# Performance work log

Hardware: AMD Instinct MI355X
Metric: run time of the kernel (lower is better)

## Reference

```python
import jax, jax.numpy as jnp
import numpy as np

B, S, D, H, FACTOR = 1, 2048, 1024, 16, 16
HD = D // H


def setup_inputs() -> dict:
    key = jax.random.key(0)
    ks = jax.random.split(key, 9)
    s = 1.0 / np.sqrt(D)
    u = lambda k, shape: jax.random.uniform(k, shape, jnp.float32, -s, s)
    return {
        "x": jax.random.normal(ks[0], (B, S, D), jnp.float32),
        "Wq": u(ks[1], (D, D)), "bq": u(ks[2], (D,)),
        "Wk": u(ks[3], (D, D)), "bk": u(ks[4], (D,)),
        "Wv": u(ks[5], (D, D)), "bv": u(ks[6], (D,)),
        "Wo": u(ks[7], (D, D)), "bo": u(ks[8], (D,)),
    }


def reference(x, Wq, bq, Wk, bk, Wv, bv, Wo, bo):
    b, s, d = x.shape
    h, hd = H, HD
    # projections -> [b, h, s, hd]
    q = (x @ Wq + bq).reshape(b, s, h, hd).transpose(0, 2, 1, 3)
    k = (x @ Wk + bk).reshape(b, s, h, hd).transpose(0, 2, 1, 3)
    v = (x @ Wv + bv).reshape(b, s, h, hd).transpose(0, 2, 1, 3)
    # dense scores [b, h, s, s]
    scores = jnp.einsum('bhqd,bhkd->bhqk', q, k) / np.sqrt(hd).astype(np.float32)
    # top-k along last dim, scatter into zeros (non-topk entries stay 0, as in torch code)
    vals, idx = jax.lax.top_k(scores, FACTOR)  # [b,h,s,FACTOR]
    flat_scores = scores.reshape(-1, s)
    rows = jnp.arange(flat_scores.shape[0])[:, None]
    sparse = jnp.zeros_like(flat_scores).at[rows, idx.reshape(-1, FACTOR)].set(
        vals.reshape(-1, FACTOR)).reshape(scores.shape)
    attn = jax.nn.softmax(sparse, axis=-1)  # softmax over sparse scores incl. zeros
    out = jnp.einsum('bhqk,bhkd->bhqd', attn, v)
    out = out.transpose(0, 2, 1, 3).reshape(b, s, d)
    return out @ Wo + bo
```

## Files before the change

kernel.cpp:

```cpp
#include <hip/hip_runtime.h>
#include <stdint.h>

constexpr int SEQ  = 2048;
constexpr int DIM  = 1024;
constexpr int NH   = 16;
constexpr int HDIM = 64;
constexpr int TOPK = 16;
constexpr int CAP  = 96;
constexpr int CST  = 97;
constexpr int QR   = 32;

typedef unsigned short bf16_t;
typedef __attribute__((ext_vector_type(8))) short bf16x8;
typedef __attribute__((ext_vector_type(4))) float f32x4;
typedef unsigned long long u64;

__device__ __forceinline__ int swzc(int col, int row) { return col ^ ((row & 7) << 3); }

__device__ __forceinline__ float bf2f(bf16_t b) {
  return __uint_as_float(((unsigned)b) << 16);
}
__device__ __forceinline__ bf16_t f2bf(float f) {
  unsigned u = __float_as_uint(f);
  unsigned r = u + 0x7fffu + ((u >> 16) & 1u);
  return (bf16_t)(r >> 16);
}
__device__ __forceinline__ f32x4 zero4() {
  f32x4 z; z[0] = 0.f; z[1] = 0.f; z[2] = 0.f; z[3] = 0.f; return z;
}
__device__ __forceinline__ void gload_lds16(const bf16_t* g, bf16_t* l) {
  __builtin_amdgcn_global_load_lds(
      (const __attribute__((address_space(1))) void*)g,
      (__attribute__((address_space(3))) void*)l, 16, 0, 0);
}
__device__ __forceinline__ unsigned ordf(float f) {
  unsigned b = __float_as_uint(f);
  return (b & 0x80000000u) ? ~b : (b | 0x80000000u);
}
__device__ __forceinline__ float iordf(unsigned u) {
  unsigned b = (u & 0x80000000u) ? (u ^ 0x80000000u) : ~u;
  return __uint_as_float(b);
}

__global__ void prep_kernel(const float* __restrict__ x, bf16_t* __restrict__ xb,
                            const float* __restrict__ W0, const float* __restrict__ W1,
                            const float* __restrict__ W2, const float* __restrict__ W3,
                            bf16_t* __restrict__ T0, bf16_t* __restrict__ T1,
                            bf16_t* __restrict__ T2, bf16_t* __restrict__ T3) {
  const int z = blockIdx.z;
  if (z == 4) {
    int bl = blockIdx.y * 32 + blockIdx.x;
    int tt = threadIdx.y * 32 + threadIdx.x;
    int i = (bl * 256 + tt) * 8;
    float4 v0 = *reinterpret_cast<const float4*>(x + i);
    float4 v1 = *reinterpret_cast<const float4*>(x + i + 4);
    bf16x8 o;
    o[0] = (short)f2bf(v0.x); o[1] = (short)f2bf(v0.y);
    o[2] = (short)f2bf(v0.z); o[3] = (short)f2bf(v0.w);
    o[4] = (short)f2bf(v1.x); o[5] = (short)f2bf(v1.y);
    o[6] = (short)f2bf(v1.z); o[7] = (short)f2bf(v1.w);
    *reinterpret_cast<bf16x8*>(xb + i) = o;
    return;
  }
  const float* W = (z == 0) ? W0 : (z == 1) ? W1 : (z == 2) ? W2 : W3;
  bf16_t* WT = (z == 0) ? T0 : (z == 1) ? T1 : (z == 2) ? T2 : T3;
  __shared__ float tile[32][33];
  int tx = threadIdx.x, ty = threadIdx.y;
  int bx = blockIdx.x * 32, by = blockIdx.y * 32;
#pragma unroll
  for (int i = 0; i < 4; ++i)
    tile[ty + i * 8][tx] = W[(by + ty + i * 8) * DIM + bx + tx];
  __syncthreads();
#pragma unroll
  for (int i = 0; i < 4; ++i)
    WT[(bx + ty + i * 8) * DIM + by + tx] = f2bf(tile[tx][ty + i * 8]);
}

__global__ __launch_bounds__(256) void gemm_qkv(const bf16_t* __restrict__ A,
                                                const bf16_t* __restrict__ B0,
                                                const bf16_t* __restrict__ B1,
                                                const bf16_t* __restrict__ B2,
                                                const float* __restrict__ c0,
                                                const float* __restrict__ c1,
                                                const float* __restrict__ c2,
                                                bf16_t* __restrict__ o0,
                                                bf16_t* __restrict__ o1,
                                                bf16_t* __restrict__ o2,
                                                float* __restrict__ sumv) {
  __shared__ __align__(16) bf16_t As[2][128 * 64];
  __shared__ __align__(16) bf16_t Bs[2][128 * 64];
  const int t = threadIdx.x;
  const int which = blockIdx.x >> 3;
  const bf16_t* Bt = (which == 0) ? B0 : (which == 1) ? B1 : B2;
  const float* bias = (which == 0) ? c0 : (which == 1) ? c1 : c2;
  bf16_t* out = (which == 0) ? o0 : (which == 1) ? o1 : o2;
  const int bm0 = blockIdx.y * 128, bn0 = (blockIdx.x & 7) * 128;
  const int w = t >> 6, lane = t & 63, lr = lane & 15, lg = lane >> 4;
  const int wm = w >> 1, wn = w & 1;
  const int srow = t >> 3;
  const int scol = swzc((t & 7) * 8, srow);
  const int ldst = srow * 64 + (t & 7) * 8;
  const int rsw = (lr & 7) << 3;

  f32x4 acc[4][4];
#pragma unroll
  for (int m = 0; m < 4; ++m)
#pragma unroll
    for (int n = 0; n < 4; ++n) acc[m][n] = zero4();

#define STAGE_G(buf, kt)                                                             \
  do {                                                                               \
    _Pragma("unroll") for (int i_ = 0; i_ < 4; ++i_) {                               \
      gload_lds16(A + (size_t)(bm0 + i_ * 32 + srow) * DIM + (kt) * 64 + scol,       \
                  &As[buf][i_ * 32 * 64 + ldst]);                                    \
      gload_lds16(Bt + (size_t)(bn0 + i_ * 32 + srow) * DIM + (kt) * 64 + scol,      \
                  &Bs[buf][i_ * 32 * 64 + ldst]);                                    \
    }                                                                                \
  } while (0)

  STAGE_G(0, 0);
  __syncthreads();

  for (int s = 0; s < 16; ++s) {
    const int cur = s & 1;
    if (s < 15) STAGE_G(cur ^ 1, s + 1);
    bf16x8 a[4][2], b[4][2];
#pragma unroll
    for (int m = 0; m < 4; ++m)
#pragma unroll
      for (int kk = 0; kk < 2; ++kk)
        a[m][kk] = *reinterpret_cast<const bf16x8*>(
            &As[cur][(wm * 64 + m * 16 + lr) * 64 + ((kk * 32 + lg * 8) ^ rsw)]);
#pragma unroll
    for (int n = 0; n < 4; ++n)
#pragma unroll
      for (int kk = 0; kk < 2; ++kk)
        b[n][kk] = *reinterpret_cast<const bf16x8*>(
            &Bs[cur][(wn * 64 + n * 16 + lr) * 64 + ((kk * 32 + lg * 8) ^ rsw)]);
#pragma unroll
    for (int m = 0; m < 4; ++m)
#pragma unroll
      for (int n = 0; n < 4; ++n)
#pragma unroll
        for (int kk = 0; kk < 2; ++kk)
          acc[m][n] = __builtin_amdgcn_mfma_f32_16x16x32_bf16(a[m][kk], b[n][kk],
                                                              acc[m][n], 0, 0, 0);
    __syncthreads();
  }
#undef STAGE_G

#pragma unroll
  for (int n = 0; n < 4; ++n) {
    int col = bn0 + wn * 64 + n * 16 + lr;
    float bv = bias[col];
    float colsum = 0.f;
#pragma unroll
    for (int m = 0; m < 4; ++m)
#pragma unroll
      for (int r = 0; r < 4; ++r) {
        int row = bm0 + wm * 64 + m * 16 + lg * 4 + r;
        bf16_t rb = f2bf(acc[m][n][r] + bv);
        out[(size_t)row * DIM + col] = rb;
        if (which == 2) colsum += bf2f(rb);
      }
    if (which == 2) atomicAdd(&sumv[col], colsum);
  }
}

__global__ __launch_bounds__(256) void gemm_wo(const bf16_t* __restrict__ A,
                                               const bf16_t* __restrict__ Bt,
                                               const float* __restrict__ bias,
                                               float* __restrict__ out) {
  __shared__ __align__(16) bf16_t As[2][128 * 64];
  __shared__ __align__(16) bf16_t Bs[2][64 * 64];
  const int t = threadIdx.x;
  const int bm0 = blockIdx.y * 128, bn0 = blockIdx.x * 64;
  const int w = t >> 6, lane = t & 63, lr = lane & 15, lg = lane >> 4;
  const int wm = w >> 1, wn = w & 1;
  const int srow = t >> 3;
  const int scol = swzc((t & 7) * 8, srow);
  const int ldst = srow * 64 + (t & 7) * 8;
  const int rsw = (lr & 7) << 3;

  f32x4 acc[4][2];
#pragma unroll
  for (int m = 0; m < 4; ++m)
#pragma unroll
    for (int n = 0; n < 2; ++n) acc[m][n] = zero4();

#define STAGE_W(buf, kt)                                                             \
  do {                                                                               \
    _Pragma("unroll") for (int i_ = 0; i_ < 4; ++i_)                                 \
      gload_lds16(A + (size_t)(bm0 + i_ * 32 + srow) * DIM + (kt) * 64 + scol,       \
                  &As[buf][i_ * 32 * 64 + ldst]);                                    \
    _Pragma("unroll") for (int i_ = 0; i_ < 2; ++i_)                                 \
      gload_lds16(Bt + (size_t)(bn0 + i_ * 32 + srow) * DIM + (kt) * 64 + scol,      \
                  &Bs[buf][i_ * 32 * 64 + ldst]);                                    \
  } while (0)

  STAGE_W(0, 0);
  __syncthreads();

  for (int s = 0; s < 16; ++s) {
    const int cur = s & 1;
    if (s < 15) STAGE_W(cur ^ 1, s + 1);
    bf16x8 a[4][2], b[2][2];
#pragma unroll
    for (int m = 0; m < 4; ++m)
#pragma unroll
      for (int kk = 0; kk < 2; ++kk)
        a[m][kk] = *reinterpret_cast<const bf16x8*>(
            &As[cur][(wm * 64 + m * 16 + lr) * 64 + ((kk * 32 + lg * 8) ^ rsw)]);
#pragma unroll
    for (int n = 0; n < 2; ++n)
#pragma unroll
      for (int kk = 0; kk < 2; ++kk)
        b[n][kk] = *reinterpret_cast<const bf16x8*>(
            &Bs[cur][(wn * 32 + n * 16 + lr) * 64 + ((kk * 32 + lg * 8) ^ rsw)]);
#pragma unroll
    for (int m = 0; m < 4; ++m)
#pragma unroll
      for (int n = 0; n < 2; ++n)
#pragma unroll
        for (int kk = 0; kk < 2; ++kk)
          acc[m][n] = __builtin_amdgcn_mfma_f32_16x16x32_bf16(a[m][kk], b[n][kk],
                                                              acc[m][n], 0, 0, 0);
    __syncthreads();
  }
#undef STAGE_W

#pragma unroll
  for (int n = 0; n < 2; ++n) {
    int col = bn0 + wn * 32 + n * 16 + lr;
    float bv = bias[col];
#pragma unroll
    for (int m = 0; m < 4; ++m)
#pragma unroll
      for (int r = 0; r < 4; ++r) {
        int row = bm0 + wm * 64 + m * 16 + lg * 4 + r;
        out[(size_t)row * DIM + col] = acc[m][n][r] + bv;
      }
  }
}

#define LOADK(buf, kc)                                                              \
  do {                                                                              \
    _Pragma("unroll") for (int n_ = 0; n_ < 4; ++n_)                                \
      _Pragma("unroll") for (int k_ = 0; k_ < 2; ++k_)                              \
        kf[buf][n_][k_] = *reinterpret_cast<const bf16x8*>(                         \
            kp + (size_t)((kc) * 64 + n_ * 16 + lr) * DIM + k_ * 32 + lg * 8);      \
  } while (0)

__global__ __launch_bounds__(256, 2) void attn_kernel(const bf16_t* __restrict__ q,
                                                      const bf16_t* __restrict__ k,
                                                      const bf16_t* __restrict__ v,
                                                      const float* __restrict__ sumv,
                                                      bf16_t* __restrict__ op) {
  __shared__ float CM[QR * 33];
  __shared__ float Tsh[QR];
  __shared__ float zsh[QR];
  __shared__ int   cnt[QR];
  __shared__ float cval[QR * CST];
  __shared__ unsigned short cidx[QR * CST];

  const int t = threadIdx.x;
  const int lin = blockIdx.x;
  const int xcd = lin & 7, ixd = lin >> 3;
  const int h = xcd * 2 + (ixd >> 6), qt = ixd & 63;
  const int w = t >> 6, lane = t & 63, lr = lane & 15, lg = lane >> 4;

  const bf16_t* qp = q + (size_t)(qt * QR) * DIM + h * HDIM;
  const bf16_t* kp = k + h * HDIM;

  bf16x8 aq[2][2];
#pragma unroll
  for (int m = 0; m < 2; ++m)
#pragma unroll
    for (int kk = 0; kk < 2; ++kk)
      aq[m][kk] = *reinterpret_cast<const bf16x8*>(
          qp + (size_t)(m * 16 + lr) * DIM + kk * 32 + lg * 8);

  bf16x8 kf[2][4][2];

  LOADK(0, w * 8);
#pragma unroll
  for (int i = 0; i < 8; ++i) {
    if (i < 7) LOADK((i + 1) & 1, w * 8 + i + 1);
    const int cur = i & 1;
    f32x4 sacc[2][4];
#pragma unroll
    for (int m = 0; m < 2; ++m)
#pragma unroll
      for (int n = 0; n < 4; ++n) sacc[m][n] = zero4();
#pragma unroll
    for (int m = 0; m < 2; ++m)
#pragma unroll
      for (int n = 0; n < 4; ++n)
#pragma unroll
        for (int kk = 0; kk < 2; ++kk)
          sacc[m][n] = __builtin_amdgcn_mfma_f32_16x16x32_bf16(kf[cur][n][kk], aq[m][kk],
                                                               sacc[m][n], 0, 0, 0);
#pragma unroll
    for (int m = 0; m < 2; ++m) {
      float mx = sacc[m][0][0];
#pragma unroll
      for (int n = 0; n < 4; ++n)
#pragma unroll
        for (int r = 0; r < 4; ++r) mx = fmaxf(mx, sacc[m][n][r]);
      mx = fmaxf(mx, __shfl_xor(mx, 16));
      mx = fmaxf(mx, __shfl_xor(mx, 32));
      if (lane < 16) CM[(m * 16 + lane) * 33 + (w * 8 + i)] = mx * 0.125f;
    }
  }
  LOADK(0, w * 8);
  __syncthreads();

  {
    const int trow = t >> 3, tsub = t & 7;
    float cmv[4];
#pragma unroll
    for (int c = 0; c < 4; ++c) cmv[c] = CM[trow * 33 + tsub * 4 + c];
    float Tval = -1e30f;
#pragma unroll
    for (int it = 0; it < TOPK; ++it) {
      float lm = fmaxf(fmaxf(cmv[0], cmv[1]), fmaxf(cmv[2], cmv[3]));
      float gm = fmaxf(lm, __shfl_xor(lm, 1));
      gm = fmaxf(gm, __shfl_xor(gm, 2));
      gm = fmaxf(gm, __shfl_xor(gm, 4));
      u64 b = __ballot(lm == gm);
      int base = lane & ~7;
      int ownsub = __ffsll((b >> base) & 0xFFull) - 1;
      if (tsub == ownsub) {
        bool d = false;
#pragma unroll
        for (int c = 0; c < 4; ++c)
          if (!d && cmv[c] == lm) { cmv[c] = -1e30f; d = true; }
      }
      Tval = gm;
    }
    if (tsub == 0) { Tsh[trow] = Tval; cnt[trow] = 0; }
  }
  __syncthreads();

  float Treg[2];
#pragma unroll
  for (int m = 0; m < 2; ++m) Treg[m] = Tsh[m * 16 + lr];

#pragma unroll
  for (int i = 0; i < 8; ++i) {
    if (i < 7) LOADK((i + 1) & 1, w * 8 + i + 1);
    const int cur = i & 1;
    const int kc = w * 8 + i;
    f32x4 sacc[2][4];
#pragma unroll
    for (int m = 0; m < 2; ++m)
#pragma unroll
      for (int n = 0; n < 4; ++n) sacc[m][n] = zero4();
#pragma unroll
    for (int m = 0; m < 2; ++m)
#pragma unroll
      for (int n = 0; n < 4; ++n)
#pragma unroll
        for (int kk = 0; kk < 2; ++kk)
          sacc[m][n] = __builtin_amdgcn_mfma_f32_16x16x32_bf16(kf[cur][n][kk], aq[m][kk],
                                                               sacc[m][n], 0, 0, 0);
#pragma unroll
    for (int m = 0; m < 2; ++m)
#pragma unroll
      for (int n = 0; n < 4; ++n)
#pragma unroll
        for (int r = 0; r < 4; ++r) {
          float val = sacc[m][n][r] * 0.125f;
          if (val >= Treg[m]) {
            int row = m * 16 + lr;
            int p = atomicAdd(&cnt[row], 1);
            if (p < CAP) {
              cval[row * CST + p] = val;
              cidx[row * CST + p] = (unsigned short)(kc * 64 + n * 16 + lg * 4 + r);
            }
          }
        }
  }
  __syncthreads();

  {
    const int trow = t >> 3, tsub = t & 7;
    int nc = cnt[trow]; if (nc > CAP) nc = CAP;
    float Zexp = 0.f;
    for (int sel = 0; sel < TOPK; ++sel) {
      u64 lmax = 0ull; int lp = -1;
      for (int p = tsub; p < nc; p += 8) {
        float vv = cval[trow * CST + p];
        unsigned id = cidx[trow * CST + p];
        u64 key = ((u64)ordf(vv) << 32) | (u64)(unsigned)(~id);
        if (key > lmax) { lmax = key; lp = p; }
      }
      u64 g = lmax;
#pragma unroll
      for (int d = 1; d < 8; d <<= 1) {
        u64 o = __shfl_xor(g, d);
        g = (o > g) ? o : g;
      }
      if (lmax == g && lp >= 0) cval[trow * CST + lp] = -1e30f;
      float val = iordf((unsigned)(g >> 32));
      int idx = (int)(~(unsigned)(g & 0xffffffffull));
      float e = expf(val);
      Zexp += e;
      if (tsub == 0) {
        CM[trow * 33 + sel] = e - 1.f;
        CM[trow * 33 + 16 + sel] = __int_as_float(idx);
      }
    }
    if (tsub == 0) zsh[trow] = 2032.f + Zexp;
  }
  __syncthreads();

  {
    const int row = t >> 3;
    const int dbase = h * HDIM + (t & 7) * 8;
    float oacc[8];
    const float4* sp = reinterpret_cast<const float4*>(sumv + dbase);
    float4 s0 = sp[0], s1 = sp[1];
    oacc[0] = s0.x; oacc[1] = s0.y; oacc[2] = s0.z; oacc[3] = s0.w;
    oacc[4] = s1.x; oacc[5] = s1.y; oacc[6] = s1.z; oacc[7] = s1.w;
    float invZ = 1.f / zsh[row];
#pragma unroll
    for (int j = 0; j < TOPK; ++j) {
      float wj = CM[row * 33 + j];
      int kidx = __float_as_int(CM[row * 33 + 16 + j]);
      bf16x8 vv = *reinterpret_cast<const bf16x8*>(v + (size_t)kidx * DIM + dbase);
#pragma unroll
      for (int e = 0; e < 8; ++e) oacc[e] += wj * bf2f((bf16_t)vv[e]);
    }
    bf16x8 o0;
#pragma unroll
    for (int e = 0; e < 8; ++e) o0[e] = (short)f2bf(oacc[e] * invZ);
    *reinterpret_cast<bf16x8*>(op + (size_t)(qt * QR + row) * DIM + dbase) = o0;
  }
}

extern "C" void kernel_launch(void* const* d_in, const int* in_sizes, int n_in,
                              void* d_out, int out_size, void* d_ws, size_t ws_size,
                              hipStream_t stream) {
  const float* x  = (const float*)d_in[0];
  const float* Wq = (const float*)d_in[1];
  const float* bq = (const float*)d_in[2];
  const float* Wk = (const float*)d_in[3];
  const float* bk = (const float*)d_in[4];
  const float* Wv = (const float*)d_in[5];
  const float* bv = (const float*)d_in[6];
  const float* Wo = (const float*)d_in[7];
  const float* bo = (const float*)d_in[8];
  float* out = (float*)d_out;

  char* ws = (char*)d_ws;
  bf16_t* xb   = (bf16_t*)(ws + (size_t)(0)  * (1 << 20));
  bf16_t* WqT  = (bf16_t*)(ws + (size_t)(4)  * (1 << 20));
  bf16_t* WkT  = (bf16_t*)(ws + (size_t)(6)  * (1 << 20));
  bf16_t* WvT  = (bf16_t*)(ws + (size_t)(8)  * (1 << 20));
  bf16_t* WoT  = (bf16_t*)(ws + (size_t)(10) * (1 << 20));
  bf16_t* qb   = (bf16_t*)(ws + (size_t)(12) * (1 << 20));
  bf16_t* kb   = (bf16_t*)(ws + (size_t)(16) * (1 << 20));
  bf16_t* vb   = (bf16_t*)(ws + (size_t)(20) * (1 << 20));
  bf16_t* opb  = (bf16_t*)(ws + (size_t)(24) * (1 << 20));
  float*  sumv = (float*) (ws + (size_t)(28) * (1 << 20));

  prep_kernel<<<dim3(32, 32, 5), dim3(32, 8), 0, stream>>>(x, xb, Wq, Wk, Wv, Wo,
                                                           WqT, WkT, WvT, WoT);
  hipMemsetAsync(sumv, 0, DIM * sizeof(float), stream);

  gemm_qkv<<<dim3(24, 16), 256, 0, stream>>>(xb, WqT, WkT, WvT, bq, bk, bv,
                                             qb, kb, vb, sumv);

  attn_kernel<<<1024, 256, 0, stream>>>(qb, kb, vb, sumv, opb);

  gemm_wo<<<dim3(16, 16), 256, 0, stream>>>(opb, WoT, bo, out);
}
```

Before: 232.3 us.

## Double query rows per attention block to halve K-tile reloads

Raises the number of query rows per attention workgroup from 32 to 64 and halves the grid to 512 blocks. Each K tile loaded from memory now feeds twice as many MFMA row tiles, and the top-k selection and output loops are remapped to 4 threads per row instead of 8. The aim is to cut redundant K reads, which are recomputed twice per block. The cost is more accumulator registers (sacc 4x4), so occupancy under launch_bounds(256,2) may drop, and there is less thread parallelism in the per-row selection phases.

```diff
diff --git a/kernel.cpp b/kernel.cpp
--- a/kernel.cpp
+++ b/kernel.cpp
@@ -8,7 +8,7 @@
 constexpr int TOPK = 16;
 constexpr int CAP  = 96;
 constexpr int CST  = 97;
-constexpr int QR   = 32;
+constexpr int QR   = 64;
 
 typedef unsigned short bf16_t;
 typedef __attribute__((ext_vector_type(8))) short bf16x8;
@@ -266,15 +266,15 @@
   const int t = threadIdx.x;
   const int lin = blockIdx.x;
   const int xcd = lin & 7, ixd = lin >> 3;
-  const int h = xcd * 2 + (ixd >> 6), qt = ixd & 63;
+  const int h = xcd * 2 + (ixd >> 5), qt = ixd & 31;
   const int w = t >> 6, lane = t & 63, lr = lane & 15, lg = lane >> 4;
 
   const bf16_t* qp = q + (size_t)(qt * QR) * DIM + h * HDIM;
   const bf16_t* kp = k + h * HDIM;
 
-  bf16x8 aq[2][2];
-#pragma unroll
-  for (int m = 0; m < 2; ++m)
+  bf16x8 aq[4][2];
+#pragma unroll
+  for (int m = 0; m < 4; ++m)
 #pragma unroll
     for (int kk = 0; kk < 2; ++kk)
       aq[m][kk] = *reinterpret_cast<const bf16x8*>(
@@ -287,13 +287,13 @@
   for (int i = 0; i < 8; ++i) {
     if (i < 7) LOADK((i + 1) & 1, w * 8 + i + 1);
     const int cur = i & 1;
-    f32x4 sacc[2][4];
-#pragma unroll
-    for (int m = 0; m < 2; ++m)
+    f32x4 sacc[4][4];
+#pragma unroll
+    for (int m = 0; m < 4; ++m)
 #pragma unroll
       for (int n = 0; n < 4; ++n) sacc[m][n] = zero4();
 #pragma unroll
-    for (int m = 0; m < 2; ++m)
+    for (int m = 0; m < 4; ++m)
 #pragma unroll
       for (int n = 0; n < 4; ++n)
 #pragma unroll
@@ -301,7 +301,7 @@
           sacc[m][n] = __builtin_amdgcn_mfma_f32_16x16x32_bf16(kf[cur][n][kk], aq[m][kk],
                                                                sacc[m][n], 0, 0, 0);
 #pragma unroll
-    for (int m = 0; m < 2; ++m) {
+    for (int m = 0; m < 4; ++m) {
       float mx = sacc[m][0][0];
 #pragma unroll
       for (int n = 0; n < 4; ++n)
@@ -316,24 +316,25 @@
   __syncthreads();
 
   {
-    const int trow = t >> 3, tsub = t & 7;
-    float cmv[4];
-#pragma unroll
-    for (int c = 0; c < 4; ++c) cmv[c] = CM[trow * 33 + tsub * 4 + c];
+    const int trow = t >> 2, tsub = t & 3;
+    float cmv[8];
+#pragma unroll
+    for (int c = 0; c < 8; ++c) cmv[c] = CM[trow * 33 + tsub * 8 + c];
     float Tval = -1e30f;
 #pragma unroll
     for (int it = 0; it < TOPK; ++it) {
-      float lm = fmaxf(fmaxf(cmv[0], cmv[1]), fmaxf(cmv[2], cmv[3]));
+      float lm = cmv[0];
+#pragma unroll
+      for (int c = 1; c < 8; ++c) lm = fmaxf(lm, cmv[c]);
       float gm = fmaxf(lm, __shfl_xor(lm, 1));
       gm = fmaxf(gm, __shfl_xor(gm, 2));
-      gm = fmaxf(gm, __shfl_xor(gm, 4));
       u64 b = __ballot(lm == gm);
-      int base = lane & ~7;
-      int ownsub = __ffsll((b >> base) & 0xFFull) - 1;
+      int base = lane & ~3;
+      int ownsub = __ffsll((b >> base) & 0xFull) - 1;
       if (tsub == ownsub) {
         bool d = false;
 #pragma unroll
-        for (int c = 0; c < 4; ++c)
+        for (int c = 0; c < 8; ++c)
           if (!d && cmv[c] == lm) { cmv[c] = -1e30f; d = true; }
       }
       Tval = gm;
@@ -342,22 +343,22 @@
   }
   __syncthreads();
 
-  float Treg[2];
-#pragma unroll
-  for (int m = 0; m < 2; ++m) Treg[m] = Tsh[m * 16 + lr];
+  float Treg[4];
+#pragma unroll
+  for (int m = 0; m < 4; ++m) Treg[m] = Tsh[m * 16 + lr];
 
 #pragma unroll
   for (int i = 0; i < 8; ++i) {
     if (i < 7) LOADK((i + 1) & 1, w * 8 + i + 1);
     const int cur = i & 1;
     const int kc = w * 8 + i;
-    f32x4 sacc[2][4];
-#pragma unroll
-    for (int m = 0; m < 2; ++m)
+    f32x4 sacc[4][4];
+#pragma unroll
+    for (int m = 0; m < 4; ++m)
 #pragma unroll
       for (int n = 0; n < 4; ++n) sacc[m][n] = zero4();
 #pragma unroll
-    for (int m = 0; m < 2; ++m)
+    for (int m = 0; m < 4; ++m)
 #pragma unroll
       for (int n = 0; n < 4; ++n)
 #pragma unroll
@@ -365,7 +366,7 @@
           sacc[m][n] = __builtin_amdgcn_mfma_f32_16x16x32_bf16(kf[cur][n][kk], aq[m][kk],
                                                                sacc[m][n], 0, 0, 0);
 #pragma unroll
-    for (int m = 0; m < 2; ++m)
+    for (int m = 0; m < 4; ++m)
 #pragma unroll
       for (int n = 0; n < 4; ++n)
 #pragma unroll
@@ -384,12 +385,12 @@
   __syncthreads();
 
   {
-    const int trow = t >> 3, tsub = t & 7;
+    const int trow = t >> 2, tsub = t & 3;
     int nc = cnt[trow]; if (nc > CAP) nc = CAP;
     float Zexp = 0.f;
     for (int sel = 0; sel < TOPK; ++sel) {
       u64 lmax = 0ull; int lp = -1;
-      for (int p = tsub; p < nc; p += 8) {
+      for (int p = tsub; p < nc; p += 4) {
         float vv = cval[trow * CST + p];
         unsigned id = cidx[trow * CST + p];
         u64 key = ((u64)ordf(vv) << 32) | (u64)(unsigned)(~id);
@@ -397,7 +398,7 @@
       }
       u64 g = lmax;
 #pragma unroll
-      for (int d = 1; d < 8; d <<= 1) {
+      for (int d = 1; d < 4; d <<= 1) {
         u64 o = __shfl_xor(g, d);
         g = (o > g) ? o : g;
       }
@@ -416,26 +417,38 @@
   __syncthreads();
 
   {
-    const int row = t >> 3;
-    const int dbase = h * HDIM + (t & 7) * 8;
-    float oacc[8];
+    const int row = t >> 2;
+    const int dbase = h * HDIM + (t & 3) * 16;
+    float oacc[16];
     const float4* sp = reinterpret_cast<const float4*>(sumv + dbase);
-    float4 s0 = sp[0], s1 = sp[1];
-    oacc[0] = s0.x; oacc[1] = s0.y; oacc[2] = s0.z; oacc[3] = s0.w;
-    oacc[4] = s1.x; oacc[5] = s1.y; oacc[6] = s1.z; oacc[7] = s1.w;
+#pragma unroll
+    for (int u = 0; u < 4; ++u) {
+      float4 s4 = sp[u];
+      oacc[u * 4 + 0] = s4.x; oacc[u * 4 + 1] = s4.y;
+      oacc[u * 4 + 2] = s4.z; oacc[u * 4 + 3] = s4.w;
+    }
     float invZ = 1.f / zsh[row];
 #pragma unroll
     for (int j = 0; j < TOPK; ++j) {
       float wj = CM[row * 33 + j];
       int kidx = __float_as_int(CM[row * 33 + 16 + j]);
-      bf16x8 vv = *reinterpret_cast<const bf16x8*>(v + (size_t)kidx * DIM + dbase);
-#pragma unroll
-      for (int e = 0; e < 8; ++e) oacc[e] += wj * bf2f((bf16_t)vv[e]);
-    }
-    bf16x8 o0;
-#pragma unroll
-    for (int e = 0; e < 8; ++e) o0[e] = (short)f2bf(oacc[e] * invZ);
-    *reinterpret_cast<bf16x8*>(op + (size_t)(qt * QR + row) * DIM + dbase) = o0;
+      const bf16x8* vp = reinterpret_cast<const bf16x8*>(v + (size_t)kidx * DIM + dbase);
+      bf16x8 v0 = vp[0], v1 = vp[1];
+#pragma unroll
+      for (int e = 0; e < 8; ++e) {
+        oacc[e] += wj * bf2f((bf16_t)v0[e]);
+        oacc[8 + e] += wj * bf2f((bf16_t)v1[e]);
+      }
+    }
+    bf16x8 o0, o1;
+#pragma unroll
+    for (int e = 0; e < 8; ++e) {
+      o0[e] = (short)f2bf(oacc[e] * invZ);
+      o1[e] = (short)f2bf(oacc[8 + e] * invZ);
+    }
+    bf16_t* orow = op + (size_t)(qt * QR + row) * DIM + dbase;
+    *reinterpret_cast<bf16x8*>(orow) = o0;
+    *reinterpret_cast<bf16x8*>(orow + 8) = o1;
   }
 }
 
@@ -472,7 +485,7 @@
   gemm_qkv<<<dim3(24, 16), 256, 0, stream>>>(xb, WqT, WkT, WvT, bq, bk, bv,
                                              qb, kb, vb, sumv);
 
-  attn_kernel<<<1024, 256, 0, stream>>>(qb, kb, vb, sumv, opb);
+  attn_kernel<<<512, 256, 0, stream>>>(qb, kb, vb, sumv, opb);
 
   gemm_wo<<<dim3(16, 16), 256, 0, stream>>>(opb, WoT, bo, out);
 }
```

Result: faster. 213.1 us (-8.3%).
